# Performance work log

Measured on AMD Instinct MI355X. Metric: run time of the kernel, lower is better.

## Reference

```python
import jax, jax.numpy as jnp
import numpy as np

B, T, D, U = 128, 1024, 512, 512  # batch, time, input dim, num_cells


def setup_inputs() -> dict:
    key = jax.random.key(0)
    ks = jax.random.split(key, 6)
    scale_in = 1.0 / np.sqrt(D)
    scale_h = 1.0 / np.sqrt(U)
    return {
        "o_inputs": jax.random.normal(ks[0], (B, T, D), dtype=jnp.float32),
        "kernel": jax.random.normal(ks[1], (D, 4 * U), dtype=jnp.float32) * scale_in,
        "recurrent_kernel": jax.random.normal(ks[2], (U, 4 * U), dtype=jnp.float32) * scale_h,
        "bias": jnp.zeros((4 * U,), dtype=jnp.float32).at[U:2 * U].set(1.0),  # unit_forget_bias
        "dense_kernel": jax.random.normal(ks[3], (2 * U, 1), dtype=jnp.float32) * (1.0 / np.sqrt(2 * U)),
        "dense_bias": jnp.zeros((1,), dtype=jnp.float32),
    }


def _skip_lstm(o_inputs, kernel, recurrent_kernel, bias, dense_kernel, dense_bias):
    batch = o_inputs.shape[0]
    units = recurrent_kernel.shape[0]

    def step(carry, x_t):
        h, c, ut = carry                      # h,c: [B,U], ut: [B]
        ug = jnp.round(ut)                    # binary skip gate
        # Keras LSTMCell: gates in i, f, g(c), o order
        z = x_t @ kernel + h @ recurrent_kernel + bias   # [B, 4U]
        i, f, g, o = jnp.split(z, 4, axis=1)
        c_n = jax.nn.sigmoid(f) * c + jax.nn.sigmoid(i) * jnp.tanh(g)
        h_n = jax.nn.sigmoid(o) * jnp.tanh(c_n)
        out = h_n                              # TensorArray stores raw cell output
        ug1 = ug[:, None]
        hb = ug1 * h + (1.0 - ug1) * h_n       # blended state
        cb = ug1 * c + (1.0 - ug1) * c_n
        delta = jax.nn.sigmoid(jnp.concatenate([hb, cb], axis=1) @ dense_kernel + dense_bias)[:, 0]
        ut_n = ug * delta + (1.0 - ug) * (ut + jnp.minimum(delta, 1.0 - ut))
        return (hb, cb, ut_n), out

    h0 = jnp.zeros((batch, units), dtype=o_inputs.dtype)
    c0 = jnp.zeros((batch, units), dtype=o_inputs.dtype)
    u0 = jnp.ones((batch,), dtype=o_inputs.dtype)
    xs = jnp.transpose(o_inputs, (1, 0, 2))   # [T,B,D]
    _, outs = jax.lax.scan(step, (h0, c0, u0), xs)
    return jnp.transpose(outs, (1, 0, 2))      # [B,T,U]


def reference(o_inputs, kernel, recurrent_kernel, bias, dense_kernel, dense_bias):
    return _skip_lstm(o_inputs, kernel, recurrent_kernel, bias, dense_kernel, dense_bias)
```

## Files before the change

### kernel.cpp

```cpp
#include <hip/hip_runtime.h>
#include <hip/hip_fp16.h>
#include <hip/hip_cooperative_groups.h>

namespace cg = cooperative_groups;

constexpr int B_ = 128, T_ = 1024, D_ = 512, U_ = 512;
constexpr int NBLK = 256, NTHR = 1024;
constexpr int G4 = 4 * U_;

__device__ __forceinline__ float sigm(float v) { return 1.0f / (1.0f + expf(-v)); }

#define AGENT_LD(p)    __hip_atomic_load((p), __ATOMIC_RELAXED, __HIP_MEMORY_SCOPE_AGENT)
#define AGENT_ST(p, v) __hip_atomic_store((p), (v), __ATOMIC_RELAXED, __HIP_MEMORY_SCOPE_AGENT)

template <typename ZT> __device__ __forceinline__ ZT    to_zt(float v);
template <> __device__ __forceinline__ float  to_zt<float>(float v)  { return v; }
template <> __device__ __forceinline__ __half to_zt<__half>(float v) { return __float2half(v); }
__device__ __forceinline__ float from_zt(float v)  { return v; }
__device__ __forceinline__ float from_zt(__half v) { return __half2float(v); }

__global__ __launch_bounds__(256) void transpose_x(const float* __restrict__ x,
                                                   float* __restrict__ xT)
{
    __shared__ float tile[32][33];
    const int tileId = blockIdx.x;
    const int bt = tileId & 3;
    const int kt = (tileId >> 2) & 15;
    const int t  = tileId >> 6;
    const int tx = threadIdx.x & 31;
    const int ty = threadIdx.x >> 5;
    #pragma unroll
    for (int r = 0; r < 4; ++r) {
        const int b = bt * 32 + ty + r * 8;
        const int k = kt * 32 + tx;
        tile[ty + r * 8][tx] = x[(size_t)b * (T_ * D_) + (size_t)t * D_ + k];
    }
    __syncthreads();
    #pragma unroll
    for (int r = 0; r < 4; ++r) {
        const int k = kt * 32 + ty + r * 8;
        const int b = bt * 32 + tx;
        xT[((size_t)t * D_ + k) * B_ + b] = tile[tx][ty + r * 8];
    }
}

__global__ __launch_bounds__(1024) void pack_w(const float* __restrict__ wk,
                                               const float* __restrict__ wr,
                                               float* __restrict__ Wpk)
{
    const size_t idx = (size_t)blockIdx.x * 1024 + threadIdx.x;
    const int    c   = (int)(idx & 7);
    const size_t k   = (idx >> 3) & 1023;
    const int    blk = (int)(idx >> 13);
    const int    col = ((c >> 1) << 9) + blk * 2 + (c & 1);
    Wpk[idx] = (k < 512) ? wk[k * G4 + col] : wr[(k - 512) * G4 + col];
}

template <typename ZT>
__global__ __launch_bounds__(NTHR, 4) void zx_gemm(
    const float* __restrict__ xT, const float* __restrict__ Wpk,
    const float* __restrict__ bias, ZT* __restrict__ zx)
{
    __shared__ float parts[8][128][9];
    __shared__ float bias_l[8];
    const int tid = threadIdx.x, blk = blockIdx.x, u0 = blk * 2;
    if (tid < 8) bias_l[tid] = bias[(tid >> 1) * U_ + u0 + (tid & 1)];
    const int b = tid & 127, ksub = tid >> 7;
    const int ksub_u = __builtin_amdgcn_readfirstlane(ksub);
    const float* __restrict__ wp = Wpk + ((size_t)blk * 1024 + (size_t)ksub_u * 64) * 8;
    __syncthreads();

    for (int t = 0; t < T_; ++t) {
        const float* __restrict__ xp = xT + ((size_t)t * D_ + ksub * 64) * B_ + b;
        float acc[8] = {0.f,0.f,0.f,0.f,0.f,0.f,0.f,0.f};
        #pragma unroll 2
        for (int kq = 0; kq < 16; ++kq) {
            const float v0 = xp[(kq * 4 + 0) * B_];
            const float v1 = xp[(kq * 4 + 1) * B_];
            const float v2 = xp[(kq * 4 + 2) * B_];
            const float v3 = xp[(kq * 4 + 3) * B_];
            const float* __restrict__ w = wp + kq * 32;
            #pragma unroll
            for (int c = 0; c < 8; ++c)
                acc[c] += v0 * w[c] + v1 * w[8 + c] + v2 * w[16 + c] + v3 * w[24 + c];
        }
        #pragma unroll
        for (int c = 0; c < 8; ++c) parts[ksub][b][c] = acc[c];
        __syncthreads();
        {
            const int c = tid >> 7, bb = tid & 127;
            float s = bias_l[c];
            #pragma unroll
            for (int ks = 0; ks < 8; ++ks) s += parts[ks][bb][c];
            zx[((size_t)t * G4 + (c >> 1) * U_ + u0 + (c & 1)) * B_ + bb] = to_zt<ZT>(s);
        }
        __syncthreads();
    }
}

template <typename ZT>
__global__ __launch_bounds__(NTHR, 4) void skiplstm_loop(
    const ZT* __restrict__ zx, const float* __restrict__ Wpk,
    const float* __restrict__ dk, const float* __restrict__ dbp,
    float* __restrict__ out, float* __restrict__ hbuf,
    float* __restrict__ pd, unsigned* __restrict__ bar)
{
    __shared__ float parts[8][128][9];
    __shared__ float pdpart[8][128];
    __shared__ float c_state[128][2];
    __shared__ float h_state[128][2];
    __shared__ float ut_lds[128];
    __shared__ float dk_l[4];
    __shared__ float db_l;

    const int tid = threadIdx.x;
    const int blk = blockIdx.x;
    const int u0  = blk * 2;

    if (tid < 2) { dk_l[tid] = dk[u0 + tid]; dk_l[2 + tid] = dk[U_ + u0 + tid]; }
    if (tid == 0) db_l = dbp[0];
    if (tid < 128) {
        ut_lds[tid] = 1.0f;
        c_state[tid][0] = 0.f; c_state[tid][1] = 0.f;
        h_state[tid][0] = 0.f; h_state[tid][1] = 0.f;
    }
    __syncthreads();

    const int b    = tid & 127;
    const int ksub = tid >> 7;
    const int ksub_u = __builtin_amdgcn_readfirstlane(ksub);
    const float* __restrict__ wp = Wpk + ((size_t)blk * 1024 + 512 + (size_t)ksub_u * 64) * 8;

    unsigned tgt = 0;
    #pragma unroll 1
    for (int t = 0; t < T_; ++t) {
        const float* __restrict__ hcur = hbuf + (t & 1) * (U_ * B_);
        float* __restrict__ hnxt = hbuf + ((t + 1) & 1) * (U_ * B_);

        const float* __restrict__ hp = hcur + (size_t)(ksub * 64) * B_ + b;
        float acc[8] = {0.f,0.f,0.f,0.f,0.f,0.f,0.f,0.f};
        #pragma unroll 2
        for (int kq = 0; kq < 16; ++kq) {
            const float v0 = AGENT_LD(hp + (kq * 4 + 0) * B_);
            const float v1 = AGENT_LD(hp + (kq * 4 + 1) * B_);
            const float v2 = AGENT_LD(hp + (kq * 4 + 2) * B_);
            const float v3 = AGENT_LD(hp + (kq * 4 + 3) * B_);
            const float* __restrict__ w = wp + kq * 32;
            #pragma unroll
            for (int c = 0; c < 8; ++c)
                acc[c] += v0 * w[c] + v1 * w[8 + c] + v2 * w[16 + c] + v3 * w[24 + c];
        }
        #pragma unroll
        for (int c = 0; c < 8; ++c) parts[ksub][b][c] = acc[c];
        __syncthreads();

        if (tid < 256) {
            const int bb = tid >> 1, j = tid & 1;
            float z[4];
            #pragma unroll
            for (int g = 0; g < 4; ++g) {
                float s = from_zt(zx[((size_t)t * G4 + g * U_ + u0 + j) * B_ + bb]);
                #pragma unroll
                for (int ks = 0; ks < 8; ++ks) s += parts[ks][bb][g * 2 + j];
                z[g] = s;
            }
            const float ut    = ut_lds[bb];
            const float ug    = rintf(ut);
            const float c_old = c_state[bb][j];
            const float si = sigm(z[0]);
            const float sf = sigm(z[1]);
            const float gg = tanhf(z[2]);
            const float so = sigm(z[3]);
            const float c_n = sf * c_old + si * gg;
            const float h_n = so * tanhf(c_n);
            const float h_old = h_state[bb][j];
            const float hbv = ug * h_old + (1.f - ug) * h_n;
            const float cbv = ug * c_old + (1.f - ug) * c_n;
            out[(size_t)bb * (T_ * U_) + (size_t)t * U_ + u0 + j] = h_n;
            AGENT_ST(hnxt + (size_t)(u0 + j) * B_ + bb, hbv);
            c_state[bb][j] = cbv;
            h_state[bb][j] = hbv;
            float p = hbv * dk_l[j] + cbv * dk_l[2 + j];
            p += __shfl_xor(p, 1);
            if (j == 0) AGENT_ST(pd + (t & 1) * (NBLK * B_) + blk * B_ + bb, p);
        }
        __syncthreads();

        tgt += NBLK;
        if (tid == 0) {
            __hip_atomic_fetch_add(bar, 1u, __ATOMIC_RELAXED, __HIP_MEMORY_SCOPE_AGENT);
            while (__hip_atomic_load(bar, __ATOMIC_RELAXED, __HIP_MEMORY_SCOPE_AGENT) < tgt)
                __builtin_amdgcn_s_sleep(2);
        }
        __syncthreads();

        {
            const int o2  = tid >> 7;
            const int bb2 = tid & 127;
            const float* __restrict__ pdt = pd + (t & 1) * (NBLK * B_);
            float s = 0.f;
            #pragma unroll 4
            for (int i = 0; i < 32; ++i)
                s += AGENT_LD(pdt + (size_t)(o2 * 32 + i) * B_ + bb2);
            pdpart[o2][bb2] = s;
        }
        __syncthreads();
        if (tid < 128) {
            float ss = 0.f;
            #pragma unroll
            for (int o = 0; o < 8; ++o) ss += pdpart[o][tid];
            const float delta = sigm(ss + db_l);
            const float ut = ut_lds[tid];
            const float ug = rintf(ut);
            ut_lds[tid] = ug * delta + (1.f - ug) * (ut + fminf(delta, 1.f - ut));
        }
    }
}

__global__ __launch_bounds__(NTHR, 4) void skiplstm_kernel_T(
    const float* __restrict__ xT, const float* __restrict__ wk,
    const float* __restrict__ wr, const float* __restrict__ bias,
    const float* __restrict__ dk, const float* __restrict__ dbp,
    float* __restrict__ out, float* __restrict__ hbuf, float* __restrict__ pd)
{
    __shared__ __align__(16) float Wlds[8][1024];
    __shared__ float parts[8][128][9];
    __shared__ float c_state[128][2];
    __shared__ float ut_lds[128];
    __shared__ float bias_l[8];
    __shared__ float dk_l[4];
    __shared__ float db_l;

    const int tid = threadIdx.x;
    const int u0 = blockIdx.x * 2;

    #pragma unroll
    for (int c = 0; c < 8; ++c) {
        const int g = c >> 1, j = c & 1;
        const int gcol = g * U_ + u0 + j;
        Wlds[c][tid] = (tid < D_) ? wk[(size_t)tid * G4 + gcol]
                                  : wr[(size_t)(tid - D_) * G4 + gcol];
    }
    if (tid < 8)  bias_l[tid] = bias[(tid >> 1) * U_ + u0 + (tid & 1)];
    if (tid < 2) { dk_l[tid] = dk[u0 + tid]; dk_l[2 + tid] = dk[U_ + u0 + tid]; }
    if (tid == 0) db_l = dbp[0];
    if (tid < 128) { ut_lds[tid] = 1.0f; c_state[tid][0] = 0.0f; c_state[tid][1] = 0.0f; }
    if (tid < 512) hbuf[blockIdx.x * 512 + tid] = 0.0f;

    cg::grid_group grid = cg::this_grid();
    __syncthreads();
    grid.sync();

    const int b    = tid & 127;
    const int ksub = tid >> 7;

    #pragma unroll 1
    for (int t = 0; t < T_; ++t) {
        const float* __restrict__ hcurT = hbuf + (t & 1) * (U_ * B_);
        float* __restrict__ hnxtT = hbuf + ((t + 1) & 1) * (U_ * B_);

        const float* __restrict__ src = (ksub < 4)
            ? (xT + ((size_t)t * D_ + ksub * 128) * B_ + b)
            : (hcurT + (size_t)(ksub - 4) * 128 * B_ + b);

        float acc[8] = {0.f,0.f,0.f,0.f,0.f,0.f,0.f,0.f};
        #pragma unroll 2
        for (int kq = 0; kq < 32; ++kq) {
            const float v0 = src[(kq * 4 + 0) * B_];
            const float v1 = src[(kq * 4 + 1) * B_];
            const float v2 = src[(kq * 4 + 2) * B_];
            const float v3 = src[(kq * 4 + 3) * B_];
            const int k4 = ksub * 32 + kq;
            #pragma unroll
            for (int c = 0; c < 8; ++c) {
                const float4 w = ((const float4*)(&Wlds[c][0]))[k4];
                acc[c] += v0 * w.x + v1 * w.y + v2 * w.z + v3 * w.w;
            }
        }
        #pragma unroll
        for (int c = 0; c < 8; ++c) parts[ksub][b][c] = acc[c];
        __syncthreads();

        if (tid < 256) {
            const int bb = tid >> 1, j = tid & 1;
            float z[4];
            #pragma unroll
            for (int g = 0; g < 4; ++g) {
                float s = bias_l[g*2 + j];
                #pragma unroll
                for (int ks = 0; ks < 8; ++ks) s += parts[ks][bb][g*2 + j];
                z[g] = s;
            }
            const float ut    = ut_lds[bb];
            const float ug    = rintf(ut);
            const float c_old = c_state[bb][j];
            const float si = sigm(z[0]);
            const float sf = sigm(z[1]);
            const float gg = tanhf(z[2]);
            const float so = sigm(z[3]);
            const float c_n = sf * c_old + si * gg;
            const float h_n = so * tanhf(c_n);
            const float h_old = hcurT[(u0 + j) * B_ + bb];
            const float hbv = ug * h_old + (1.f - ug) * h_n;
            const float cbv = ug * c_old + (1.f - ug) * c_n;
            out[(size_t)bb * (T_ * U_) + (size_t)t * U_ + u0 + j] = h_n;
            hnxtT[(u0 + j) * B_ + bb] = hbv;
            c_state[bb][j] = cbv;
            float p = hbv * dk_l[j] + cbv * dk_l[2 + j];
            p += __shfl_xor(p, 1);
            if (j == 0) pd[(t & 1) * (NBLK * B_) + blockIdx.x * B_ + bb] = p;
        }

        grid.sync();

        {
            const int bb2 = tid >> 3, o = tid & 7;
            const float* __restrict__ pdt = pd + (t & 1) * (NBLK * B_);
            float s = 0.f;
            #pragma unroll 1
            for (int i = 0; i < 32; ++i) s += pdt[(o * 32 + i) * B_ + bb2];
            s += __shfl_xor(s, 1);
            s += __shfl_xor(s, 2);
            s += __shfl_xor(s, 4);
            if (o == 0) {
                const float delta = sigm(s + db_l);
                const float ut = ut_lds[bb2];
                const float ug = rintf(ut);
                ut_lds[bb2] = ug * delta + (1.f - ug) * (ut + fminf(delta, 1.f - ut));
            }
        }
        __syncthreads();
    }
}

extern "C" void kernel_launch(void* const* d_in, const int* in_sizes, int n_in,
                              void* d_out, int out_size, void* d_ws, size_t ws_size,
                              hipStream_t stream)
{
    (void)in_sizes; (void)n_in; (void)out_size;
    const float* x  = (const float*)d_in[0];
    const float* wk = (const float*)d_in[1];
    const float* wr = (const float*)d_in[2];
    const float* bs = (const float*)d_in[3];
    const float* dk = (const float*)d_in[4];
    const float* db = (const float*)d_in[5];
    float* out = (float*)d_out;

    const size_t xT_b   = (size_t)T_ * D_ * B_ * 4;
    const size_t wpk_b  = (size_t)NBLK * 1024 * 8 * 4;
    const size_t hbuf_b = (size_t)2 * U_ * B_ * 4;
    const size_t pd_b   = (size_t)2 * NBLK * B_ * 4;
    const size_t zx32_b = (size_t)T_ * G4 * B_ * 4;
    const size_t zx16_b = zx32_b / 2;
    const size_t tail_b = hbuf_b + pd_b + 256;

    const size_t need_A = zx32_b + xT_b + wpk_b + tail_b;
    const size_t need_B = zx16_b + xT_b + wpk_b + tail_b;
    const size_t need_C = xT_b + hbuf_b + pd_b;

    char* w = (char*)d_ws;

    if (ws_size >= need_B) {
        const bool f32zx = (ws_size >= need_A);
        const size_t zx_b = f32zx ? zx32_b : zx16_b;
        char* zxp  = w;
        float* xT  = (float*)(w + zx_b);
        float* Wpk = (float*)(w + zx_b + xT_b);
        float* hbuf = (float*)(w + zx_b + xT_b + wpk_b);
        float* pd   = (float*)(w + zx_b + xT_b + wpk_b + hbuf_b);
        unsigned* bar = (unsigned*)(w + zx_b + xT_b + wpk_b + hbuf_b + pd_b);

        hipMemsetAsync(hbuf, 0, hbuf_b + pd_b + 256, stream);
        transpose_x<<<dim3(T_ * 16 * 4), dim3(256), 0, stream>>>(x, xT);
        pack_w<<<dim3(2048), dim3(1024), 0, stream>>>(wk, wr, Wpk);

        if (f32zx) {
            float* zx = (float*)zxp;
            zx_gemm<float><<<dim3(NBLK), dim3(NTHR), 0, stream>>>(xT, Wpk, bs, zx);
            void* args[] = { (void*)&zx, (void*)&Wpk, (void*)&dk, (void*)&db,
                             (void*)&out, (void*)&hbuf, (void*)&pd, (void*)&bar };
            hipLaunchCooperativeKernel(reinterpret_cast<void*>(skiplstm_loop<float>),
                                       dim3(NBLK), dim3(NTHR), args, 0, stream);
        } else {
            __half* zx = (__half*)zxp;
            zx_gemm<__half><<<dim3(NBLK), dim3(NTHR), 0, stream>>>(xT, Wpk, bs, zx);
            void* args[] = { (void*)&zx, (void*)&Wpk, (void*)&dk, (void*)&db,
                             (void*)&out, (void*)&hbuf, (void*)&pd, (void*)&bar };
            hipLaunchCooperativeKernel(reinterpret_cast<void*>(skiplstm_loop<__half>),
                                       dim3(NBLK), dim3(NTHR), args, 0, stream);
        }
    } else {
        float* xT   = (float*)d_ws;
        float* hbuf = xT + (size_t)T_ * D_ * B_;
        float* pd   = hbuf + 2 * U_ * B_;
        transpose_x<<<dim3(T_ * 16 * 4), dim3(256), 0, stream>>>(x, xT);
        void* args[] = { (void*)&xT, (void*)&wk, (void*)&wr, (void*)&bs, (void*)&dk, (void*)&db,
                         (void*)&out, (void*)&hbuf, (void*)&pd };
        hipLaunchCooperativeKernel(reinterpret_cast<void*>(skiplstm_kernel_T),
                                   dim3(NBLK), dim3(NTHR), args, 0, stream);
        (void)need_C;
    }
}
```

Before: 22.47 ms.

## Use hierarchical grid barrier and offload delta reduction to dedicated blocks

Replaces the single global atomic counter barrier with a two-level barrier (16 groups of 16 blocks feeding a root counter) to cut contention on one address. The redundant per-block reduction of the dense-layer partials across all 256 blocks is replaced by 16 reducer blocks that compute delta and publish it with a ready counter. The ut update moves into the next step's gate computation, which waits on that counter. Also prefetches the zx value and all 64 h values into registers before the FMA loop. Risks include higher register pressure from the 64-element array and an extra spin-wait on the critical path.

```diff
diff --git a/kernel.cpp b/kernel.cpp
--- a/kernel.cpp
+++ b/kernel.cpp
@@ -7,6 +7,8 @@
 constexpr int B_ = 128, T_ = 1024, D_ = 512, U_ = 512;
 constexpr int NBLK = 256, NTHR = 1024;
 constexpr int G4 = 4 * U_;
+constexpr int NGRP = 16, GRPSZ = 16;
+constexpr int NRED = 16;
 
 __device__ __forceinline__ float sigm(float v) { return 1.0f / (1.0f + expf(-v)); }
 
@@ -103,10 +105,11 @@
     const ZT* __restrict__ zx, const float* __restrict__ Wpk,
     const float* __restrict__ dk, const float* __restrict__ dbp,
     float* __restrict__ out, float* __restrict__ hbuf,
-    float* __restrict__ pd, unsigned* __restrict__ bar)
+    float* __restrict__ pd, unsigned* __restrict__ ctrl)
 {
     __shared__ float parts[8][128][9];
-    __shared__ float pdpart[8][128];
+    __shared__ float zxl[8][128];
+    __shared__ float red[8][132];
     __shared__ float c_state[128][2];
     __shared__ float h_state[128][2];
     __shared__ float ut_lds[128];
@@ -116,6 +119,11 @@
     const int tid = threadIdx.x;
     const int blk = blockIdx.x;
     const int u0  = blk * 2;
+
+    unsigned* __restrict__ bar_grp  = ctrl;
+    unsigned* __restrict__ bar_root = ctrl + 256;
+    unsigned* __restrict__ dready   = ctrl + 272;
+    float*    __restrict__ delta_g  = (float*)(ctrl + 288);
 
     if (tid < 2) { dk_l[tid] = dk[u0 + tid]; dk_l[2 + tid] = dk[U_ + u0 + tid]; }
     if (tid == 0) db_l = dbp[0];
@@ -130,48 +138,61 @@
     const int ksub = tid >> 7;
     const int ksub_u = __builtin_amdgcn_readfirstlane(ksub);
     const float* __restrict__ wp = Wpk + ((size_t)blk * 1024 + 512 + (size_t)ksub_u * 64) * 8;
-
-    unsigned tgt = 0;
+    const int g = blk >> 4;
+
     #pragma unroll 1
     for (int t = 0; t < T_; ++t) {
         const float* __restrict__ hcur = hbuf + (t & 1) * (U_ * B_);
         float* __restrict__ hnxt = hbuf + ((t + 1) & 1) * (U_ * B_);
 
+        const ZT zreg = zx[((size_t)t * G4 + (ksub >> 1) * U_ + u0 + (ksub & 1)) * B_ + b];
+
         const float* __restrict__ hp = hcur + (size_t)(ksub * 64) * B_ + b;
+        float hv[64];
+        #pragma unroll
+        for (int i = 0; i < 64; ++i) hv[i] = AGENT_LD(hp + i * B_);
+
         float acc[8] = {0.f,0.f,0.f,0.f,0.f,0.f,0.f,0.f};
-        #pragma unroll 2
+        #pragma unroll
         for (int kq = 0; kq < 16; ++kq) {
-            const float v0 = AGENT_LD(hp + (kq * 4 + 0) * B_);
-            const float v1 = AGENT_LD(hp + (kq * 4 + 1) * B_);
-            const float v2 = AGENT_LD(hp + (kq * 4 + 2) * B_);
-            const float v3 = AGENT_LD(hp + (kq * 4 + 3) * B_);
             const float* __restrict__ w = wp + kq * 32;
             #pragma unroll
             for (int c = 0; c < 8; ++c)
-                acc[c] += v0 * w[c] + v1 * w[8 + c] + v2 * w[16 + c] + v3 * w[24 + c];
+                acc[c] += hv[4*kq+0] * w[c]      + hv[4*kq+1] * w[8 + c]
+                        + hv[4*kq+2] * w[16 + c] + hv[4*kq+3] * w[24 + c];
         }
         #pragma unroll
         for (int c = 0; c < 8; ++c) parts[ksub][b][c] = acc[c];
+        zxl[ksub][b] = from_zt(zreg);
         __syncthreads();
 
         if (tid < 256) {
             const int bb = tid >> 1, j = tid & 1;
+            float ut, ug;
+            if (t == 0) { ut = 1.0f; ug = 1.0f; }
+            else {
+                const unsigned tgt_d = (unsigned)(NRED * t);
+                while (AGENT_LD(dready) < tgt_d) __builtin_amdgcn_s_sleep(1);
+                const float dlt = AGENT_LD(delta_g + ((t - 1) & 1) * 128 + bb);
+                const float utp = ut_lds[bb];
+                const float ugp = rintf(utp);
+                ut = ugp * dlt + (1.f - ugp) * (utp + fminf(dlt, 1.f - utp));
+                ug = rintf(ut);
+            }
             float z[4];
             #pragma unroll
-            for (int g = 0; g < 4; ++g) {
-                float s = from_zt(zx[((size_t)t * G4 + g * U_ + u0 + j) * B_ + bb]);
+            for (int gg4 = 0; gg4 < 4; ++gg4) {
+                float s = zxl[gg4 * 2 + j][bb];
                 #pragma unroll
-                for (int ks = 0; ks < 8; ++ks) s += parts[ks][bb][g * 2 + j];
-                z[g] = s;
-            }
-            const float ut    = ut_lds[bb];
-            const float ug    = rintf(ut);
+                for (int ks = 0; ks < 8; ++ks) s += parts[ks][bb][gg4 * 2 + j];
+                z[gg4] = s;
+            }
             const float c_old = c_state[bb][j];
             const float si = sigm(z[0]);
             const float sf = sigm(z[1]);
-            const float gg = tanhf(z[2]);
+            const float gt = tanhf(z[2]);
             const float so = sigm(z[3]);
-            const float c_n = sf * c_old + si * gg;
+            const float c_n = sf * c_old + si * gt;
             const float h_n = so * tanhf(c_n);
             const float h_old = h_state[bb][j];
             const float hbv = ug * h_old + (1.f - ug) * h_n;
@@ -182,37 +203,42 @@
             h_state[bb][j] = hbv;
             float p = hbv * dk_l[j] + cbv * dk_l[2 + j];
             p += __shfl_xor(p, 1);
-            if (j == 0) AGENT_ST(pd + (t & 1) * (NBLK * B_) + blk * B_ + bb, p);
-        }
-        __syncthreads();
-
-        tgt += NBLK;
+            if (j == 0) {
+                AGENT_ST(pd + (t & 1) * (NBLK * B_) + blk * B_ + bb, p);
+                ut_lds[bb] = ut;
+            }
+        }
+        __syncthreads();
+
         if (tid == 0) {
-            __hip_atomic_fetch_add(bar, 1u, __ATOMIC_RELAXED, __HIP_MEMORY_SCOPE_AGENT);
-            while (__hip_atomic_load(bar, __ATOMIC_RELAXED, __HIP_MEMORY_SCOPE_AGENT) < tgt)
-                __builtin_amdgcn_s_sleep(2);
-        }
-        __syncthreads();
-
-        {
-            const int o2  = tid >> 7;
-            const int bb2 = tid & 127;
+            const unsigned old = __hip_atomic_fetch_add(bar_grp + g * 16, 1u,
+                                    __ATOMIC_RELEASE, __HIP_MEMORY_SCOPE_AGENT);
+            if (old + 1u == (unsigned)(GRPSZ * (t + 1)))
+                __hip_atomic_fetch_add(bar_root, 1u,
+                                    __ATOMIC_RELEASE, __HIP_MEMORY_SCOPE_AGENT);
+            const unsigned tgt = (unsigned)(NGRP * (t + 1));
+            while (__hip_atomic_load(bar_root, __ATOMIC_RELAXED, __HIP_MEMORY_SCOPE_AGENT) < tgt)
+                __builtin_amdgcn_s_sleep(1);
+        }
+        __syncthreads();
+
+        if (blk < NRED && t < T_ - 1) {
+            const int b8 = tid & 7, i = tid >> 3;
+            const int bg = blk * 8 + b8;
             const float* __restrict__ pdt = pd + (t & 1) * (NBLK * B_);
-            float s = 0.f;
-            #pragma unroll 4
-            for (int i = 0; i < 32; ++i)
-                s += AGENT_LD(pdt + (size_t)(o2 * 32 + i) * B_ + bb2);
-            pdpart[o2][bb2] = s;
-        }
-        __syncthreads();
-        if (tid < 128) {
-            float ss = 0.f;
-            #pragma unroll
-            for (int o = 0; o < 8; ++o) ss += pdpart[o][tid];
-            const float delta = sigm(ss + db_l);
-            const float ut = ut_lds[tid];
-            const float ug = rintf(ut);
-            ut_lds[tid] = ug * delta + (1.f - ug) * (ut + fminf(delta, 1.f - ut));
+            red[b8][i] = AGENT_LD(pdt + (size_t)(i * 2 + 0) * B_ + bg)
+                       + AGENT_LD(pdt + (size_t)(i * 2 + 1) * B_ + bg);
+            __syncthreads();
+            if (tid < 8) {
+                float ss = 0.f;
+                #pragma unroll 4
+                for (int i2 = 0; i2 < 128; ++i2) ss += red[tid][i2];
+                AGENT_ST(delta_g + (t & 1) * 128 + blk * 8 + tid, sigm(ss + db_l));
+            }
+            __syncthreads();
+            if (tid == 0)
+                __hip_atomic_fetch_add(dready, 1u,
+                                    __ATOMIC_RELEASE, __HIP_MEMORY_SCOPE_AGENT);
         }
     }
 }
@@ -350,13 +376,13 @@
     const size_t wpk_b  = (size_t)NBLK * 1024 * 8 * 4;
     const size_t hbuf_b = (size_t)2 * U_ * B_ * 4;
     const size_t pd_b   = (size_t)2 * NBLK * B_ * 4;
+    const size_t ctrl_b = 4096;
     const size_t zx32_b = (size_t)T_ * G4 * B_ * 4;
     const size_t zx16_b = zx32_b / 2;
-    const size_t tail_b = hbuf_b + pd_b + 256;
+    const size_t tail_b = hbuf_b + pd_b + ctrl_b;
 
     const size_t need_A = zx32_b + xT_b + wpk_b + tail_b;
     const size_t need_B = zx16_b + xT_b + wpk_b + tail_b;
-    const size_t need_C = xT_b + hbuf_b + pd_b;
 
     char* w = (char*)d_ws;
 
@@ -368,9 +394,9 @@
         float* Wpk = (float*)(w + zx_b + xT_b);
         float* hbuf = (float*)(w + zx_b + xT_b + wpk_b);
         float* pd   = (float*)(w + zx_b + xT_b + wpk_b + hbuf_b);
-        unsigned* bar = (unsigned*)(w + zx_b + xT_b + wpk_b + hbuf_b + pd_b);
-
-        hipMemsetAsync(hbuf, 0, hbuf_b + pd_b + 256, stream);
+        unsigned* ctrl = (unsigned*)(w + zx_b + xT_b + wpk_b + hbuf_b + pd_b);
+
+        hipMemsetAsync(hbuf, 0, tail_b, stream);
         transpose_x<<<dim3(T_ * 16 * 4), dim3(256), 0, stream>>>(x, xT);
         pack_w<<<dim3(2048), dim3(1024), 0, stream>>>(wk, wr, Wpk);
 
@@ -378,14 +404,14 @@
             float* zx = (float*)zxp;
             zx_gemm<float><<<dim3(NBLK), dim3(NTHR), 0, stream>>>(xT, Wpk, bs, zx);
             void* args[] = { (void*)&zx, (void*)&Wpk, (void*)&dk, (void*)&db,
-                             (void*)&out, (void*)&hbuf, (void*)&pd, (void*)&bar };
+                             (void*)&out, (void*)&hbuf, (void*)&pd, (void*)&ctrl };
             hipLaunchCooperativeKernel(reinterpret_cast<void*>(skiplstm_loop<float>),
                                        dim3(NBLK), dim3(NTHR), args, 0, stream);
         } else {
             __half* zx = (__half*)zxp;
             zx_gemm<__half><<<dim3(NBLK), dim3(NTHR), 0, stream>>>(xT, Wpk, bs, zx);
             void* args[] = { (void*)&zx, (void*)&Wpk, (void*)&dk, (void*)&db,
-                             (void*)&out, (void*)&hbuf, (void*)&pd, (void*)&bar };
+                             (void*)&out, (void*)&hbuf, (void*)&pd, (void*)&ctrl };
             hipLaunchCooperativeKernel(reinterpret_cast<void*>(skiplstm_loop<__half>),
                                        dim3(NBLK), dim3(NTHR), args, 0, stream);
         }
@@ -398,6 +424,5 @@
                          (void*)&out, (void*)&hbuf, (void*)&pd };
         hipLaunchCooperativeKernel(reinterpret_cast<void*>(skiplstm_kernel_T),
                                    dim3(NBLK), dim3(NTHR), args, 0, stream);
-        (void)need_C;
-    }
-}
+    }
+}
```

After: 28.97 ms. +28.9%, slower.

## Split recurrent loop into two batch groups with hierarchical per-group barrier

Applied to the files above, without the earlier changes.

Repartitions the recurrent LSTM loop so each block owns 4 units for half the batch (64 rows) rather than 2 units for the full batch. The grid is split into two independent batch groups that synchronise only within themselves. A two-level atomic barrier replaces the flat 256-block counter: 16-block subgroups feed a root counter. Recurrent weights are repacked per unit-block, and zx is staged through LDS. The goal is to cut barrier contention, the cross-block delta reduction and per-block h traffic, at the cost of more LDS and register pressure from 16 accumulators per thread.

```diff
diff --git a/kernel.cpp b/kernel.cpp
--- a/kernel.cpp
+++ b/kernel.cpp
@@ -7,6 +7,7 @@
 constexpr int B_ = 128, T_ = 1024, D_ = 512, U_ = 512;
 constexpr int NBLK = 256, NTHR = 1024;
 constexpr int G4 = 4 * U_;
+constexpr int RGN = 2, RBLK = 128, RROWS = 64, UPB = 4;
 
 __device__ __forceinline__ float sigm(float v) { return 1.0f / (1.0f + expf(-v)); }
 
@@ -56,6 +57,17 @@
     Wpk[idx] = (k < 512) ? wk[k * G4 + col] : wr[(k - 512) * G4 + col];
 }
 
+__global__ __launch_bounds__(1024) void pack_w2(const float* __restrict__ wr,
+                                                float* __restrict__ Wpk2)
+{
+    const size_t idx = (size_t)blockIdx.x * 1024 + threadIdx.x;
+    const int c  = (int)(idx & 15);
+    const int k  = (int)((idx >> 4) & 511);
+    const int ub = (int)(idx >> 13);
+    const int g = c >> 2, u = c & 3;
+    Wpk2[idx] = wr[(size_t)k * G4 + g * 512 + ub * 4 + u];
+}
+
 template <typename ZT>
 __global__ __launch_bounds__(NTHR, 4) void zx_gemm(
     const float* __restrict__ xT, const float* __restrict__ Wpk,
@@ -99,120 +111,148 @@
 }
 
 template <typename ZT>
-__global__ __launch_bounds__(NTHR, 4) void skiplstm_loop(
-    const ZT* __restrict__ zx, const float* __restrict__ Wpk,
+__global__ __launch_bounds__(NTHR, 4) void skiplstm_loop2(
+    const ZT* __restrict__ zx, const float* __restrict__ Wpk2,
     const float* __restrict__ dk, const float* __restrict__ dbp,
     float* __restrict__ out, float* __restrict__ hbuf,
-    float* __restrict__ pd, unsigned* __restrict__ bar)
-{
-    __shared__ float parts[8][128][9];
-    __shared__ float pdpart[8][128];
-    __shared__ float c_state[128][2];
-    __shared__ float h_state[128][2];
-    __shared__ float ut_lds[128];
-    __shared__ float dk_l[4];
+    float* __restrict__ pd, unsigned* __restrict__ ctrl)
+{
+    __shared__ float parts[16][64][17];
+    __shared__ float zxl[16][64];
+    __shared__ float red[16][66];
+    __shared__ float pdp[4][64];
+    __shared__ float c_state[64][4];
+    __shared__ float h_state[64][4];
+    __shared__ float ut_lds[64];
+    __shared__ float dk_l[8];
     __shared__ float db_l;
 
     const int tid = threadIdx.x;
     const int blk = blockIdx.x;
-    const int u0  = blk * 2;
-
-    if (tid < 2) { dk_l[tid] = dk[u0 + tid]; dk_l[2 + tid] = dk[U_ + u0 + tid]; }
+    const int rg  = blk >> 7;
+    const int ub  = blk & 127;
+    const int rowbase = rg * RROWS;
+
+    if (tid < 4) { dk_l[tid] = dk[ub * 4 + tid]; dk_l[4 + tid] = dk[U_ + ub * 4 + tid]; }
     if (tid == 0) db_l = dbp[0];
-    if (tid < 128) {
+    if (tid < 64) {
         ut_lds[tid] = 1.0f;
-        c_state[tid][0] = 0.f; c_state[tid][1] = 0.f;
-        h_state[tid][0] = 0.f; h_state[tid][1] = 0.f;
+        #pragma unroll
+        for (int u = 0; u < 4; ++u) { c_state[tid][u] = 0.f; h_state[tid][u] = 0.f; }
     }
     __syncthreads();
 
-    const int b    = tid & 127;
-    const int ksub = tid >> 7;
-    const int ksub_u = __builtin_amdgcn_readfirstlane(ksub);
-    const float* __restrict__ wp = Wpk + ((size_t)blk * 1024 + 512 + (size_t)ksub_u * 64) * 8;
-
-    unsigned tgt = 0;
+    const int row = tid & 63;
+    const int kg  = tid >> 6;
+    const int kg_u = __builtin_amdgcn_readfirstlane(kg);
+    const float* __restrict__ wp = Wpk2 + ((size_t)ub * 512 + (size_t)kg_u * 32) * 16;
+
+    unsigned* __restrict__ grp  = ctrl + rg * 256 + (ub >> 4) * 16;
+    unsigned* __restrict__ root = ctrl + rg * 256 + 128;
+
     #pragma unroll 1
     for (int t = 0; t < T_; ++t) {
         const float* __restrict__ hcur = hbuf + (t & 1) * (U_ * B_);
         float* __restrict__ hnxt = hbuf + ((t + 1) & 1) * (U_ * B_);
 
-        const float* __restrict__ hp = hcur + (size_t)(ksub * 64) * B_ + b;
-        float acc[8] = {0.f,0.f,0.f,0.f,0.f,0.f,0.f,0.f};
-        #pragma unroll 2
-        for (int kq = 0; kq < 16; ++kq) {
-            const float v0 = AGENT_LD(hp + (kq * 4 + 0) * B_);
-            const float v1 = AGENT_LD(hp + (kq * 4 + 1) * B_);
-            const float v2 = AGENT_LD(hp + (kq * 4 + 2) * B_);
-            const float v3 = AGENT_LD(hp + (kq * 4 + 3) * B_);
-            const float* __restrict__ w = wp + kq * 32;
-            #pragma unroll
-            for (int c = 0; c < 8; ++c)
-                acc[c] += v0 * w[c] + v1 * w[8 + c] + v2 * w[16 + c] + v3 * w[24 + c];
-        }
-        #pragma unroll
-        for (int c = 0; c < 8; ++c) parts[ksub][b][c] = acc[c];
+        const int zc = kg;
+        const ZT zv = zx[((size_t)t * G4 + (zc >> 2) * U_ + ub * 4 + (zc & 3)) * B_
+                         + rowbase + row];
+
+        const float* __restrict__ hp = hcur + rowbase + row;
+        const int k0 = kg * 32;
+        float acc[16];
+        #pragma unroll
+        for (int c = 0; c < 16; ++c) acc[c] = 0.f;
+        #pragma unroll
+        for (int ii = 0; ii < 4; ++ii) {
+            float hv[8];
+            #pragma unroll
+            for (int j = 0; j < 8; ++j)
+                hv[j] = AGENT_LD(hp + (size_t)(k0 + ii * 8 + j) * B_);
+            #pragma unroll
+            for (int j = 0; j < 8; ++j) {
+                const float* __restrict__ w = wp + (ii * 8 + j) * 16;
+                #pragma unroll
+                for (int c = 0; c < 16; ++c) acc[c] += hv[j] * w[c];
+            }
+        }
+        #pragma unroll
+        for (int c = 0; c < 16; ++c) parts[kg][row][c] = acc[c];
+        zxl[zc][row] = from_zt(zv);
         __syncthreads();
 
         if (tid < 256) {
-            const int bb = tid >> 1, j = tid & 1;
+            const int u = tid >> 6, r = tid & 63;
             float z[4];
             #pragma unroll
             for (int g = 0; g < 4; ++g) {
-                float s = from_zt(zx[((size_t)t * G4 + g * U_ + u0 + j) * B_ + bb]);
+                float s = zxl[g * 4 + u][r];
                 #pragma unroll
-                for (int ks = 0; ks < 8; ++ks) s += parts[ks][bb][g * 2 + j];
+                for (int kk = 0; kk < 16; ++kk) s += parts[kk][r][g * 4 + u];
                 z[g] = s;
             }
-            const float ut    = ut_lds[bb];
-            const float ug    = rintf(ut);
-            const float c_old = c_state[bb][j];
+            const float ut = ut_lds[r];
+            const float ug = rintf(ut);
+            const float c_old = c_state[r][u];
             const float si = sigm(z[0]);
             const float sf = sigm(z[1]);
-            const float gg = tanhf(z[2]);
+            const float gt = tanhf(z[2]);
             const float so = sigm(z[3]);
-            const float c_n = sf * c_old + si * gg;
+            const float c_n = sf * c_old + si * gt;
             const float h_n = so * tanhf(c_n);
-            const float h_old = h_state[bb][j];
+            const float h_old = h_state[r][u];
             const float hbv = ug * h_old + (1.f - ug) * h_n;
             const float cbv = ug * c_old + (1.f - ug) * c_n;
-            out[(size_t)bb * (T_ * U_) + (size_t)t * U_ + u0 + j] = h_n;
-            AGENT_ST(hnxt + (size_t)(u0 + j) * B_ + bb, hbv);
-            c_state[bb][j] = cbv;
-            h_state[bb][j] = hbv;
-            float p = hbv * dk_l[j] + cbv * dk_l[2 + j];
-            p += __shfl_xor(p, 1);
-            if (j == 0) AGENT_ST(pd + (t & 1) * (NBLK * B_) + blk * B_ + bb, p);
-        }
-        __syncthreads();
-
-        tgt += NBLK;
-        if (tid == 0) {
-            __hip_atomic_fetch_add(bar, 1u, __ATOMIC_RELAXED, __HIP_MEMORY_SCOPE_AGENT);
-            while (__hip_atomic_load(bar, __ATOMIC_RELAXED, __HIP_MEMORY_SCOPE_AGENT) < tgt)
-                __builtin_amdgcn_s_sleep(2);
-        }
-        __syncthreads();
-
-        {
-            const int o2  = tid >> 7;
-            const int bb2 = tid & 127;
-            const float* __restrict__ pdt = pd + (t & 1) * (NBLK * B_);
-            float s = 0.f;
-            #pragma unroll 4
-            for (int i = 0; i < 32; ++i)
-                s += AGENT_LD(pdt + (size_t)(o2 * 32 + i) * B_ + bb2);
-            pdpart[o2][bb2] = s;
-        }
-        __syncthreads();
-        if (tid < 128) {
-            float ss = 0.f;
-            #pragma unroll
-            for (int o = 0; o < 8; ++o) ss += pdpart[o][tid];
-            const float delta = sigm(ss + db_l);
-            const float ut = ut_lds[tid];
-            const float ug = rintf(ut);
-            ut_lds[tid] = ug * delta + (1.f - ug) * (ut + fminf(delta, 1.f - ut));
+            const int b = rowbase + r, uglob = ub * 4 + u;
+            out[(size_t)b * (T_ * U_) + (size_t)t * U_ + uglob] = h_n;
+            AGENT_ST(hnxt + (size_t)uglob * B_ + b, hbv);
+            c_state[r][u] = cbv;
+            h_state[r][u] = hbv;
+            pdp[u][r] = hbv * dk_l[u] + cbv * dk_l[4 + u];
+        }
+        __syncthreads();
+        if (tid < 64) {
+            const float p = pdp[0][tid] + pdp[1][tid] + pdp[2][tid] + pdp[3][tid];
+            AGENT_ST(pd + (t & 1) * (RGN * RBLK * RROWS) + rg * (RBLK * RROWS)
+                        + ub * RROWS + tid, p);
+        }
+        __syncthreads();
+
+        if (t < T_ - 1) {
+            if (tid == 0) {
+                const unsigned old = __hip_atomic_fetch_add(grp, 1u,
+                                        __ATOMIC_RELEASE, __HIP_MEMORY_SCOPE_AGENT);
+                if (old + 1u == (unsigned)(16 * (t + 1)))
+                    __hip_atomic_fetch_add(root, 1u,
+                                        __ATOMIC_RELEASE, __HIP_MEMORY_SCOPE_AGENT);
+                const unsigned tgt = (unsigned)(8 * (t + 1));
+                while (__hip_atomic_load(root, __ATOMIC_RELAXED,
+                                         __HIP_MEMORY_SCOPE_AGENT) < tgt)
+                    __builtin_amdgcn_s_sleep(2);
+            }
+            __syncthreads();
+
+            {
+                const float* __restrict__ pdt =
+                    pd + (t & 1) * (RGN * RBLK * RROWS) + rg * (RBLK * RROWS);
+                const int i = tid >> 6, r2 = tid & 63;
+                float s = 0.f;
+                #pragma unroll
+                for (int j = 0; j < 8; ++j)
+                    s += AGENT_LD(pdt + (size_t)(i * 8 + j) * RROWS + r2);
+                red[i][r2] = s;
+            }
+            __syncthreads();
+            if (tid < 64) {
+                float ss = 0.f;
+                #pragma unroll
+                for (int i2 = 0; i2 < 16; ++i2) ss += red[i2][tid];
+                const float dlt = sigm(ss + db_l);
+                const float utv = ut_lds[tid];
+                const float ugv = rintf(utv);
+                ut_lds[tid] = ugv * dlt + (1.f - ugv) * (utv + fminf(dlt, 1.f - utv));
+            }
         }
     }
 }
@@ -348,45 +388,48 @@
 
     const size_t xT_b   = (size_t)T_ * D_ * B_ * 4;
     const size_t wpk_b  = (size_t)NBLK * 1024 * 8 * 4;
+    const size_t wpk2_b = (size_t)RBLK * 512 * 16 * 4;
     const size_t hbuf_b = (size_t)2 * U_ * B_ * 4;
-    const size_t pd_b   = (size_t)2 * NBLK * B_ * 4;
+    const size_t pd_b   = (size_t)2 * RGN * RBLK * RROWS * 4;
+    const size_t ctrl_b = 4096;
     const size_t zx32_b = (size_t)T_ * G4 * B_ * 4;
     const size_t zx16_b = zx32_b / 2;
-    const size_t tail_b = hbuf_b + pd_b + 256;
-
-    const size_t need_A = zx32_b + xT_b + wpk_b + tail_b;
-    const size_t need_B = zx16_b + xT_b + wpk_b + tail_b;
-    const size_t need_C = xT_b + hbuf_b + pd_b;
+    const size_t tail_b = hbuf_b + pd_b + ctrl_b;
+
+    const size_t need_A = zx32_b + xT_b + wpk_b + wpk2_b + tail_b;
+    const size_t need_B = zx16_b + xT_b + wpk_b + wpk2_b + tail_b;
 
     char* w = (char*)d_ws;
 
     if (ws_size >= need_B) {
         const bool f32zx = (ws_size >= need_A);
         const size_t zx_b = f32zx ? zx32_b : zx16_b;
-        char* zxp  = w;
-        float* xT  = (float*)(w + zx_b);
-        float* Wpk = (float*)(w + zx_b + xT_b);
-        float* hbuf = (float*)(w + zx_b + xT_b + wpk_b);
-        float* pd   = (float*)(w + zx_b + xT_b + wpk_b + hbuf_b);
-        unsigned* bar = (unsigned*)(w + zx_b + xT_b + wpk_b + hbuf_b + pd_b);
-
-        hipMemsetAsync(hbuf, 0, hbuf_b + pd_b + 256, stream);
+        char*  zxp  = w;
+        float* xT   = (float*)(w + zx_b);
+        float* Wpk  = (float*)(w + zx_b + xT_b);
+        float* Wpk2 = (float*)(w + zx_b + xT_b + wpk_b);
+        float* hbuf = (float*)(w + zx_b + xT_b + wpk_b + wpk2_b);
+        float* pd   = (float*)(w + zx_b + xT_b + wpk_b + wpk2_b + hbuf_b);
+        unsigned* ctrl = (unsigned*)(w + zx_b + xT_b + wpk_b + wpk2_b + hbuf_b + pd_b);
+
+        hipMemsetAsync(hbuf, 0, tail_b, stream);
         transpose_x<<<dim3(T_ * 16 * 4), dim3(256), 0, stream>>>(x, xT);
         pack_w<<<dim3(2048), dim3(1024), 0, stream>>>(wk, wr, Wpk);
+        pack_w2<<<dim3(1024), dim3(1024), 0, stream>>>(wr, Wpk2);
 
         if (f32zx) {
             float* zx = (float*)zxp;
             zx_gemm<float><<<dim3(NBLK), dim3(NTHR), 0, stream>>>(xT, Wpk, bs, zx);
-            void* args[] = { (void*)&zx, (void*)&Wpk, (void*)&dk, (void*)&db,
-                             (void*)&out, (void*)&hbuf, (void*)&pd, (void*)&bar };
-            hipLaunchCooperativeKernel(reinterpret_cast<void*>(skiplstm_loop<float>),
+            void* args[] = { (void*)&zx, (void*)&Wpk2, (void*)&dk, (void*)&db,
+                             (void*)&out, (void*)&hbuf, (void*)&pd, (void*)&ctrl };
+            hipLaunchCooperativeKernel(reinterpret_cast<void*>(skiplstm_loop2<float>),
                                        dim3(NBLK), dim3(NTHR), args, 0, stream);
         } else {
             __half* zx = (__half*)zxp;
             zx_gemm<__half><<<dim3(NBLK), dim3(NTHR), 0, stream>>>(xT, Wpk, bs, zx);
-            void* args[] = { (void*)&zx, (void*)&Wpk, (void*)&dk, (void*)&db,
-                             (void*)&out, (void*)&hbuf, (void*)&pd, (void*)&bar };
-            hipLaunchCooperativeKernel(reinterpret_cast<void*>(skiplstm_loop<__half>),
+            void* args[] = { (void*)&zx, (void*)&Wpk2, (void*)&dk, (void*)&db,
+                             (void*)&out, (void*)&hbuf, (void*)&pd, (void*)&ctrl };
+            hipLaunchCooperativeKernel(reinterpret_cast<void*>(skiplstm_loop2<__half>),
                                        dim3(NBLK), dim3(NTHR), args, 0, stream);
         }
     } else {
@@ -398,6 +441,5 @@
                          (void*)&out, (void*)&hbuf, (void*)&pd };
         hipLaunchCooperativeKernel(reinterpret_cast<void*>(skiplstm_kernel_T),
                                    dim3(NBLK), dim3(NTHR), args, 0, stream);
-        (void)need_C;
-    }
-}
+    }
+}
```

After: 24.72 ms. +10.0%, slower.

## Restructure skip-LSTM step sync with hierarchical barrier and two-level delta reduction

Applied to the files above, without the earlier changes.

Replaces the flat 256-block atomic barrier with a two-level counter barrier (groups of 16 blocks), and moves the dense-gate reduction to 16 reducer blocks that publish partial sums, which every block waits on before the next step. The recurrent matmul now uses the raw h_n broadcast and blends the recurrent pre-activation with the skip gate, instead of exchanging blended h. It also prefetches the next step's zx into LDS and loads the h/x vectors into registers up front. The fp16 zx fallback is dropped. The cost is an extra sync point per step and more register pressure from the 64-element register arrays.

```diff
diff --git a/kernel.cpp b/kernel.cpp
--- a/kernel.cpp
+++ b/kernel.cpp
@@ -1,5 +1,4 @@
 #include <hip/hip_runtime.h>
-#include <hip/hip_fp16.h>
 #include <hip/hip_cooperative_groups.h>
 
 namespace cg = cooperative_groups;
@@ -11,13 +10,8 @@
 __device__ __forceinline__ float sigm(float v) { return 1.0f / (1.0f + expf(-v)); }
 
 #define AGENT_LD(p)    __hip_atomic_load((p), __ATOMIC_RELAXED, __HIP_MEMORY_SCOPE_AGENT)
+#define AGENT_LDA(p)   __hip_atomic_load((p), __ATOMIC_ACQUIRE, __HIP_MEMORY_SCOPE_AGENT)
 #define AGENT_ST(p, v) __hip_atomic_store((p), (v), __ATOMIC_RELAXED, __HIP_MEMORY_SCOPE_AGENT)
-
-template <typename ZT> __device__ __forceinline__ ZT    to_zt(float v);
-template <> __device__ __forceinline__ float  to_zt<float>(float v)  { return v; }
-template <> __device__ __forceinline__ __half to_zt<__half>(float v) { return __float2half(v); }
-__device__ __forceinline__ float from_zt(float v)  { return v; }
-__device__ __forceinline__ float from_zt(__half v) { return __half2float(v); }
 
 __global__ __launch_bounds__(256) void transpose_x(const float* __restrict__ x,
                                                    float* __restrict__ xT)
@@ -56,10 +50,9 @@
     Wpk[idx] = (k < 512) ? wk[k * G4 + col] : wr[(k - 512) * G4 + col];
 }
 
-template <typename ZT>
 __global__ __launch_bounds__(NTHR, 4) void zx_gemm(
     const float* __restrict__ xT, const float* __restrict__ Wpk,
-    const float* __restrict__ bias, ZT* __restrict__ zx)
+    const float* __restrict__ bias, float* __restrict__ zx)
 {
     __shared__ float parts[8][128][9];
     __shared__ float bias_l[8];
@@ -72,13 +65,16 @@
 
     for (int t = 0; t < T_; ++t) {
         const float* __restrict__ xp = xT + ((size_t)t * D_ + ksub * 64) * B_ + b;
+        float xv[64];
+        #pragma unroll
+        for (int i = 0; i < 64; ++i) xv[i] = xp[(size_t)i * B_];
         float acc[8] = {0.f,0.f,0.f,0.f,0.f,0.f,0.f,0.f};
-        #pragma unroll 2
+        #pragma unroll
         for (int kq = 0; kq < 16; ++kq) {
-            const float v0 = xp[(kq * 4 + 0) * B_];
-            const float v1 = xp[(kq * 4 + 1) * B_];
-            const float v2 = xp[(kq * 4 + 2) * B_];
-            const float v3 = xp[(kq * 4 + 3) * B_];
+            const float v0 = xv[kq * 4 + 0];
+            const float v1 = xv[kq * 4 + 1];
+            const float v2 = xv[kq * 4 + 2];
+            const float v3 = xv[kq * 4 + 3];
             const float* __restrict__ w = wp + kq * 32;
             #pragma unroll
             for (int c = 0; c < 8; ++c)
@@ -92,24 +88,24 @@
             float s = bias_l[c];
             #pragma unroll
             for (int ks = 0; ks < 8; ++ks) s += parts[ks][bb][c];
-            zx[((size_t)t * G4 + (c >> 1) * U_ + u0 + (c & 1)) * B_ + bb] = to_zt<ZT>(s);
-        }
-        __syncthreads();
-    }
-}
-
-template <typename ZT>
-__global__ __launch_bounds__(NTHR, 4) void skiplstm_loop(
-    const ZT* __restrict__ zx, const float* __restrict__ Wpk,
+            zx[((size_t)t * G4 + (c >> 1) * U_ + u0 + (c & 1)) * B_ + bb] = s;
+        }
+        __syncthreads();
+    }
+}
+
+__global__ __launch_bounds__(NTHR, 4) void skiplstm_loop3(
+    const float* __restrict__ zx, const float* __restrict__ Wpk,
     const float* __restrict__ dk, const float* __restrict__ dbp,
-    float* __restrict__ out, float* __restrict__ hbuf,
-    float* __restrict__ pd, unsigned* __restrict__ bar)
+    float* __restrict__ out, float* __restrict__ hn,
+    float* __restrict__ pd, float* __restrict__ pd2, unsigned* __restrict__ ctrl)
 {
     __shared__ float parts[8][128][9];
-    __shared__ float pdpart[8][128];
-    __shared__ float c_state[128][2];
-    __shared__ float h_state[128][2];
-    __shared__ float ut_lds[128];
+    __shared__ float zxl[2][8][128];
+    __shared__ float zr[8][128];
+    __shared__ float red[8][128];
+    __shared__ float h_state[128][2], c_state[128][2];
+    __shared__ float ut_lds[128], ug_lds[128], ug_prev_lds[128];
     __shared__ float dk_l[4];
     __shared__ float db_l;
 
@@ -117,103 +113,138 @@
     const int blk = blockIdx.x;
     const int u0  = blk * 2;
 
+    for (int i = tid; i < 9216; i += NTHR) ((float*)parts)[i] = 0.f;
+    ((float*)zr)[tid & 1023] = 0.f;
+    {
+        const int c = tid >> 7, b = tid & 127;
+        zxl[0][c][b] = zx[((size_t)0 * G4 + ((c >> 1) << 9) + u0 + (c & 1)) * B_ + b];
+    }
+    if (tid < 128) {
+        ut_lds[tid] = 1.0f; ug_lds[tid] = 1.0f; ug_prev_lds[tid] = 1.0f;
+        h_state[tid][0] = 0.f; h_state[tid][1] = 0.f;
+        c_state[tid][0] = 0.f; c_state[tid][1] = 0.f;
+    }
     if (tid < 2) { dk_l[tid] = dk[u0 + tid]; dk_l[2 + tid] = dk[U_ + u0 + tid]; }
     if (tid == 0) db_l = dbp[0];
-    if (tid < 128) {
-        ut_lds[tid] = 1.0f;
-        c_state[tid][0] = 0.f; c_state[tid][1] = 0.f;
-        h_state[tid][0] = 0.f; h_state[tid][1] = 0.f;
-    }
     __syncthreads();
 
-    const int b    = tid & 127;
-    const int ksub = tid >> 7;
-    const int ksub_u = __builtin_amdgcn_readfirstlane(ksub);
-    const float* __restrict__ wp = Wpk + ((size_t)blk * 1024 + 512 + (size_t)ksub_u * 64) * 8;
-
-    unsigned tgt = 0;
+    const int bI = tid & 127, ksI = tid >> 7;
+    const int ks_u = __builtin_amdgcn_readfirstlane(ksI);
+    const float* __restrict__ wp = Wpk + ((size_t)blk * 1024 + 512 + (size_t)ks_u * 64) * 8;
+
     #pragma unroll 1
     for (int t = 0; t < T_; ++t) {
-        const float* __restrict__ hcur = hbuf + (t & 1) * (U_ * B_);
-        float* __restrict__ hnxt = hbuf + ((t + 1) & 1) * (U_ * B_);
-
-        const float* __restrict__ hp = hcur + (size_t)(ksub * 64) * B_ + b;
-        float acc[8] = {0.f,0.f,0.f,0.f,0.f,0.f,0.f,0.f};
-        #pragma unroll 2
-        for (int kq = 0; kq < 16; ++kq) {
-            const float v0 = AGENT_LD(hp + (kq * 4 + 0) * B_);
-            const float v1 = AGENT_LD(hp + (kq * 4 + 1) * B_);
-            const float v2 = AGENT_LD(hp + (kq * 4 + 2) * B_);
-            const float v3 = AGENT_LD(hp + (kq * 4 + 3) * B_);
-            const float* __restrict__ w = wp + kq * 32;
-            #pragma unroll
-            for (int c = 0; c < 8; ++c)
-                acc[c] += v0 * w[c] + v1 * w[8 + c] + v2 * w[16 + c] + v3 * w[24 + c];
-        }
-        #pragma unroll
-        for (int c = 0; c < 8; ++c) parts[ksub][b][c] = acc[c];
-        __syncthreads();
+        if (t > 0) {
+            if (tid == 0) {
+                while (AGENT_LDA(&ctrl[272]) < (unsigned)(16 * t))
+                    __builtin_amdgcn_s_sleep(1);
+            }
+            __syncthreads();
+            if (tid < 128) {
+                const float* __restrict__ p2 = pd2 + ((t - 1) & 1) * 2048;
+                float ss = 0.f;
+                #pragma unroll
+                for (int a = 0; a < 16; ++a) ss += AGENT_LD(p2 + a * 128 + tid);
+                const float dlt = sigm(ss + db_l);
+                const float utp = ut_lds[tid];
+                const float ugp = rintf(utp);
+                const float utn = ugp * dlt + (1.f - ugp) * (utp + fminf(dlt, 1.f - utp));
+                ug_prev_lds[tid] = ugp;
+                ut_lds[tid] = utn;
+                ug_lds[tid] = rintf(utn);
+            }
+            __syncthreads();
+        }
 
         if (tid < 256) {
             const int bb = tid >> 1, j = tid & 1;
+            const float ug  = ug_lds[bb];
+            const float ugp = ug_prev_lds[bb];
             float z[4];
             #pragma unroll
             for (int g = 0; g < 4; ++g) {
-                float s = from_zt(zx[((size_t)t * G4 + g * U_ + u0 + j) * B_ + bb]);
+                const int c = g * 2 + j;
+                float zn = parts[0][bb][c];
                 #pragma unroll
-                for (int ks = 0; ks < 8; ++ks) s += parts[ks][bb][g * 2 + j];
-                z[g] = s;
-            }
-            const float ut    = ut_lds[bb];
-            const float ug    = rintf(ut);
+                for (int ks = 1; ks < 8; ++ks) zn += parts[ks][bb][c];
+                const float zrn = ugp * zr[c][bb] + (1.f - ugp) * zn;
+                zr[c][bb] = zrn;
+                z[g] = zxl[t & 1][c][bb] + zrn;
+            }
             const float c_old = c_state[bb][j];
             const float si = sigm(z[0]);
             const float sf = sigm(z[1]);
-            const float gg = tanhf(z[2]);
+            const float gt = tanhf(z[2]);
             const float so = sigm(z[3]);
-            const float c_n = sf * c_old + si * gg;
+            const float c_n = sf * c_old + si * gt;
             const float h_n = so * tanhf(c_n);
             const float h_old = h_state[bb][j];
             const float hbv = ug * h_old + (1.f - ug) * h_n;
             const float cbv = ug * c_old + (1.f - ug) * c_n;
             out[(size_t)bb * (T_ * U_) + (size_t)t * U_ + u0 + j] = h_n;
-            AGENT_ST(hnxt + (size_t)(u0 + j) * B_ + bb, hbv);
+            AGENT_ST(hn + (t & 1) * (U_ * B_) + (size_t)(u0 + j) * B_ + bb, h_n);
+            h_state[bb][j] = hbv;
             c_state[bb][j] = cbv;
-            h_state[bb][j] = hbv;
             float p = hbv * dk_l[j] + cbv * dk_l[2 + j];
             p += __shfl_xor(p, 1);
             if (j == 0) AGENT_ST(pd + (t & 1) * (NBLK * B_) + blk * B_ + bb, p);
         }
         __syncthreads();
 
-        tgt += NBLK;
+        if (t == T_ - 1) break;
+
         if (tid == 0) {
-            __hip_atomic_fetch_add(bar, 1u, __ATOMIC_RELAXED, __HIP_MEMORY_SCOPE_AGENT);
-            while (__hip_atomic_load(bar, __ATOMIC_RELAXED, __HIP_MEMORY_SCOPE_AGENT) < tgt)
-                __builtin_amdgcn_s_sleep(2);
-        }
-        __syncthreads();
+            const unsigned old = __hip_atomic_fetch_add(&ctrl[(blk >> 4) * 16], 1u,
+                                    __ATOMIC_RELEASE, __HIP_MEMORY_SCOPE_AGENT);
+            if (old + 1u == (unsigned)(16 * (t + 1)))
+                __hip_atomic_fetch_add(&ctrl[256], 1u,
+                                    __ATOMIC_RELEASE, __HIP_MEMORY_SCOPE_AGENT);
+            while (AGENT_LDA(&ctrl[256]) < (unsigned)(16 * (t + 1)))
+                __builtin_amdgcn_s_sleep(1);
+        }
+        __syncthreads();
+
+        if (blk < 16) {
+            const float* __restrict__ pdt = pd + (t & 1) * (NBLK * B_);
+            const int i = tid >> 7, r = tid & 127;
+            red[i][r] = AGENT_LD(pdt + (size_t)(blk * 16 + i) * B_ + r)
+                      + AGENT_LD(pdt + (size_t)(blk * 16 + i + 8) * B_ + r);
+            __syncthreads();
+            if (tid < 128) {
+                float ss = red[0][tid];
+                #pragma unroll
+                for (int i2 = 1; i2 < 8; ++i2) ss += red[i2][tid];
+                AGENT_ST(pd2 + (t & 1) * 2048 + blk * 128 + tid, ss);
+            }
+            __syncthreads();
+            if (tid == 0)
+                __hip_atomic_fetch_add(&ctrl[272], 1u,
+                                    __ATOMIC_RELEASE, __HIP_MEMORY_SCOPE_AGENT);
+        }
 
         {
-            const int o2  = tid >> 7;
-            const int bb2 = tid & 127;
-            const float* __restrict__ pdt = pd + (t & 1) * (NBLK * B_);
-            float s = 0.f;
-            #pragma unroll 4
-            for (int i = 0; i < 32; ++i)
-                s += AGENT_LD(pdt + (size_t)(o2 * 32 + i) * B_ + bb2);
-            pdpart[o2][bb2] = s;
-        }
-        __syncthreads();
-        if (tid < 128) {
-            float ss = 0.f;
-            #pragma unroll
-            for (int o = 0; o < 8; ++o) ss += pdpart[o][tid];
-            const float delta = sigm(ss + db_l);
-            const float ut = ut_lds[tid];
-            const float ug = rintf(ut);
-            ut_lds[tid] = ug * delta + (1.f - ug) * (ut + fminf(delta, 1.f - ut));
-        }
+            const float zreg = zx[((size_t)(t + 1) * G4 + ((ksI >> 1) << 9) + u0 + (ksI & 1)) * B_ + bI];
+            const float* __restrict__ hp = hn + (t & 1) * (U_ * B_) + (size_t)(ksI * 64) * B_ + bI;
+            float hv[64];
+            #pragma unroll
+            for (int i = 0; i < 64; ++i) hv[i] = AGENT_LD(hp + (size_t)i * B_);
+            float acc[8] = {0.f,0.f,0.f,0.f,0.f,0.f,0.f,0.f};
+            #pragma unroll
+            for (int kq = 0; kq < 16; ++kq) {
+                const float v0 = hv[kq * 4 + 0];
+                const float v1 = hv[kq * 4 + 1];
+                const float v2 = hv[kq * 4 + 2];
+                const float v3 = hv[kq * 4 + 3];
+                const float* __restrict__ w = wp + kq * 32;
+                #pragma unroll
+                for (int c = 0; c < 8; ++c)
+                    acc[c] += v0 * w[c] + v1 * w[8 + c] + v2 * w[16 + c] + v3 * w[24 + c];
+            }
+            #pragma unroll
+            for (int c = 0; c < 8; ++c) parts[ksI][bI][c] = acc[c];
+            zxl[(t + 1) & 1][ksI][bI] = zreg;
+        }
+        __syncthreads();
     }
 }
 
@@ -346,49 +377,36 @@
     const float* db = (const float*)d_in[5];
     float* out = (float*)d_out;
 
+    const size_t zx_b   = (size_t)T_ * G4 * B_ * 4;
     const size_t xT_b   = (size_t)T_ * D_ * B_ * 4;
     const size_t wpk_b  = (size_t)NBLK * 1024 * 8 * 4;
-    const size_t hbuf_b = (size_t)2 * U_ * B_ * 4;
+    const size_t hn_b   = (size_t)2 * U_ * B_ * 4;
     const size_t pd_b   = (size_t)2 * NBLK * B_ * 4;
-    const size_t zx32_b = (size_t)T_ * G4 * B_ * 4;
-    const size_t zx16_b = zx32_b / 2;
-    const size_t tail_b = hbuf_b + pd_b + 256;
-
-    const size_t need_A = zx32_b + xT_b + wpk_b + tail_b;
-    const size_t need_B = zx16_b + xT_b + wpk_b + tail_b;
-    const size_t need_C = xT_b + hbuf_b + pd_b;
+    const size_t pd2_b  = (size_t)2 * 16 * 128 * 4;
+    const size_t ctrl_b = 4096;
+    const size_t tail_b = hn_b + pd_b + pd2_b + ctrl_b;
+    const size_t need   = zx_b + xT_b + wpk_b + tail_b;
 
     char* w = (char*)d_ws;
 
-    if (ws_size >= need_B) {
-        const bool f32zx = (ws_size >= need_A);
-        const size_t zx_b = f32zx ? zx32_b : zx16_b;
-        char* zxp  = w;
-        float* xT  = (float*)(w + zx_b);
-        float* Wpk = (float*)(w + zx_b + xT_b);
-        float* hbuf = (float*)(w + zx_b + xT_b + wpk_b);
-        float* pd   = (float*)(w + zx_b + xT_b + wpk_b + hbuf_b);
-        unsigned* bar = (unsigned*)(w + zx_b + xT_b + wpk_b + hbuf_b + pd_b);
-
-        hipMemsetAsync(hbuf, 0, hbuf_b + pd_b + 256, stream);
+    if (ws_size >= need) {
+        float* zxp  = (float*)w;
+        float* xT   = (float*)(w + zx_b);
+        float* Wpk  = (float*)(w + zx_b + xT_b);
+        float* hn   = (float*)(w + zx_b + xT_b + wpk_b);
+        float* pd   = (float*)(w + zx_b + xT_b + wpk_b + hn_b);
+        float* pd2  = (float*)(w + zx_b + xT_b + wpk_b + hn_b + pd_b);
+        unsigned* ctrl = (unsigned*)(w + zx_b + xT_b + wpk_b + hn_b + pd_b + pd2_b);
+
+        hipMemsetAsync(hn, 0, tail_b, stream);
         transpose_x<<<dim3(T_ * 16 * 4), dim3(256), 0, stream>>>(x, xT);
         pack_w<<<dim3(2048), dim3(1024), 0, stream>>>(wk, wr, Wpk);
-
-        if (f32zx) {
-            float* zx = (float*)zxp;
-            zx_gemm<float><<<dim3(NBLK), dim3(NTHR), 0, stream>>>(xT, Wpk, bs, zx);
-            void* args[] = { (void*)&zx, (void*)&Wpk, (void*)&dk, (void*)&db,
-                             (void*)&out, (void*)&hbuf, (void*)&pd, (void*)&bar };
-            hipLaunchCooperativeKernel(reinterpret_cast<void*>(skiplstm_loop<float>),
-                                       dim3(NBLK), dim3(NTHR), args, 0, stream);
-        } else {
-            __half* zx = (__half*)zxp;
-            zx_gemm<__half><<<dim3(NBLK), dim3(NTHR), 0, stream>>>(xT, Wpk, bs, zx);
-            void* args[] = { (void*)&zx, (void*)&Wpk, (void*)&dk, (void*)&db,
-                             (void*)&out, (void*)&hbuf, (void*)&pd, (void*)&bar };
-            hipLaunchCooperativeKernel(reinterpret_cast<void*>(skiplstm_loop<__half>),
-                                       dim3(NBLK), dim3(NTHR), args, 0, stream);
-        }
+        zx_gemm<<<dim3(NBLK), dim3(NTHR), 0, stream>>>(xT, Wpk, bs, zxp);
+
+        void* args[] = { (void*)&zxp, (void*)&Wpk, (void*)&dk, (void*)&db,
+                         (void*)&out, (void*)&hn, (void*)&pd, (void*)&pd2, (void*)&ctrl };
+        hipLaunchCooperativeKernel(reinterpret_cast<void*>(skiplstm_loop3),
+                                   dim3(NBLK), dim3(NTHR), args, 0, stream);
     } else {
         float* xT   = (float*)d_ws;
         float* hbuf = xT + (size_t)T_ * D_ * B_;
@@ -398,6 +416,5 @@
                          (void*)&out, (void*)&hbuf, (void*)&pd };
         hipLaunchCooperativeKernel(reinterpret_cast<void*>(skiplstm_kernel_T),
                                    dim3(NBLK), dim3(NTHR), args, 0, stream);
-        (void)need_C;
-    }
-}
+    }
+}
```

New measurement: 54.32 ms. 142% more time.
